# Performance work log

Hardware: AMD Instinct MI355X
Metric: run time of the kernel (lower is better)

The kernel has to match this reference:

```python
import jax, jax.numpy as jnp
import numpy as np
import math

HIDDEN = 2048
HEADS = 16
HEAD_DIM = HIDDEN // HEADS
RANK = HIDDEN // 2  # rank_ratio=0.5
B, S = 1, 4096


def setup_inputs() -> dict:
    key = jax.random.key(0)
    ks = jax.random.split(key, 10)
    sd = lambda fan_in: 1.0 / math.sqrt(fan_in)
    inp = {
        "hidden_states": jax.random.normal(ks[0], (B, S, HIDDEN), dtype=jnp.float32),
        "attention_mask": jnp.zeros((B, 1, S, S), dtype=jnp.float32),
        # low-rank projection weights; Linear weight shape is [out, in]
        "q_V": jax.random.uniform(ks[1], (RANK, HIDDEN), jnp.float32, -sd(HIDDEN), sd(HIDDEN)),
        "q_U": jax.random.uniform(ks[2], (HIDDEN, RANK), jnp.float32, -sd(RANK), sd(RANK)),
        "k_V": jax.random.uniform(ks[3], (RANK, HIDDEN), jnp.float32, -sd(HIDDEN), sd(HIDDEN)),
        "k_U": jax.random.uniform(ks[4], (HIDDEN, RANK), jnp.float32, -sd(RANK), sd(RANK)),
        "v_V": jax.random.uniform(ks[5], (RANK, HIDDEN), jnp.float32, -sd(HIDDEN), sd(HIDDEN)),
        "v_U": jax.random.uniform(ks[6], (HIDDEN, RANK), jnp.float32, -sd(RANK), sd(RANK)),
        "o_W": jax.random.uniform(ks[7], (HIDDEN, HIDDEN), jnp.float32, -sd(HIDDEN), sd(HIDDEN)),
        "o_b": jax.random.uniform(ks[8], (HIDDEN,), jnp.float32, -sd(HIDDEN), sd(HIDDEN)),
    }
    return inp


def _split_heads(x):
    # [B,S,HIDDEN] -> [B,H,S,Dh]
    b, s, _ = x.shape
    return x.reshape(b, s, HEADS, HEAD_DIM).transpose(0, 2, 1, 3)


def reference(hidden_states, attention_mask, q_V, q_U, k_V, k_U, v_V, v_U, o_W, o_b):
    # low-rank QKV: x @ V^T @ U^T
    q = _split_heads((hidden_states @ q_V.T) @ q_U.T)
    k = _split_heads((hidden_states @ k_V.T) @ k_U.T)
    v = _split_heads((hidden_states @ v_V.T) @ v_U.T)
    scores = jnp.einsum("bhqd,bhkd->bhqk", q, k) / math.sqrt(HEAD_DIM)
    scores = scores + attention_mask
    attn = jax.nn.softmax(scores, axis=-1)
    out = jnp.einsum("bhqk,bhkd->bhqd", attn, v)
    out = out.transpose(0, 2, 1, 3).reshape(hidden_states.shape[0], hidden_states.shape[1], HIDDEN)
    out = out @ o_W.T + o_b
    return out
```

## Files before the change

kernel.cpp:

```cpp
#include <hip/hip_runtime.h>

#define HIDDEN 2048
#define HEADS 16
#define HD 128
#define RANK 1024
#define SEQ 4096

typedef __bf16 bf16_t;
typedef __bf16 bf16x8 __attribute__((ext_vector_type(8)));
typedef __bf16 bf16x4 __attribute__((ext_vector_type(4)));
typedef float f32x4 __attribute__((ext_vector_type(4)));

#define MFMA_BF16(a, b, c) __builtin_amdgcn_mfma_f32_16x16x32_bf16((a), (b), (c), 0, 0, 0)

__device__ __forceinline__ void gload16(const bf16_t* g, bf16_t* l) {
  __builtin_amdgcn_global_load_lds(
      (const __attribute__((address_space(1))) unsigned int*)g,
      (__attribute__((address_space(3))) unsigned int*)l, 16, 0, 0);
}

struct CastSeg { const float* s; bf16_t* d; int n4; };
struct CastArgs { CastSeg seg[8]; };

__global__ __launch_bounds__(256) void cast_bf16_kernel(CastArgs a) {
  const int stride = gridDim.x * blockDim.x;
  const int tid0 = blockIdx.x * blockDim.x + threadIdx.x;
#pragma unroll
  for (int i = 0; i < 8; i++) {
    const float4* src = (const float4*)a.seg[i].s;
    bf16x4* dst = (bf16x4*)a.seg[i].d;
    const int n4 = a.seg[i].n4;
    for (int j = tid0; j < n4; j += stride) {
      float4 v = src[j];
      dst[j] = bf16x4{(bf16_t)v.x, (bf16_t)v.y, (bf16_t)v.z, (bf16_t)v.w};
    }
  }
}

template <int OUT_MODE>
__global__ __launch_bounds__(256) void gemm3(const bf16_t* __restrict__ A, int lda, int aOff,
                                             const bf16_t* __restrict__ W0,
                                             const bf16_t* __restrict__ W1,
                                             const bf16_t* __restrict__ W2,
                                             int nPerThird, int K,
                                             void* __restrict__ Cp, int ldc, size_t cOff,
                                             const float* __restrict__ bias, float s0,
                                             bf16_t* __restrict__ Ct) {
  __shared__ bf16_t As[128 * 32];
  __shared__ bf16_t Bs[128 * 32];
  const int tid = threadIdx.x, lane = tid & 63, wave = tid >> 6;
  const int wr = wave >> 1, wc = wave & 1, quad = lane >> 4, l15 = lane & 15;
  const int n0g = blockIdx.x * 128;
  const int third = n0g / nPerThird;
  const int n0 = n0g - third * nPerThird;
  const bf16_t* W = third == 0 ? W0 : (third == 1 ? W1 : W2);
  const bf16_t* Ab = A + (size_t)third * aOff;
  const int m0 = blockIdx.y * 128;
  const float sc = (third == 0) ? s0 : 1.f;

  f32x4 acc[4][4];
#pragma unroll
  for (int i = 0; i < 4; i++)
#pragma unroll
    for (int j = 0; j < 4; j++) acc[i][j] = f32x4{0.f, 0.f, 0.f, 0.f};

  const int KT = K >> 5;
  for (int kt = 0; kt < KT; ++kt) {
#pragma unroll
    for (int i = 0; i < 2; i++) {
      int slot = (wave * 2 + i) * 64 + lane;
      int row = slot >> 2, cp = slot & 3;
      int cl = cp ^ ((row >> 1) & 3);
      gload16(Ab + (size_t)(m0 + row) * lda + kt * 32 + cl * 8, As + (size_t)(wave * 2 + i) * 512);
    }
#pragma unroll
    for (int i = 0; i < 2; i++) {
      int slot = (wave * 2 + i) * 64 + lane;
      int row = slot >> 2, cp = slot & 3;
      int cl = cp ^ ((row >> 1) & 3);
      gload16(W + (size_t)(n0 + row) * K + kt * 32 + cl * 8, Bs + (size_t)(wave * 2 + i) * 512);
    }
    __syncthreads();

    bf16x8 af[4], bfr[4];
#pragma unroll
    for (int mt = 0; mt < 4; mt++) {
      int row = wr * 64 + mt * 16 + l15;
      int phys = quad ^ ((row >> 1) & 3);
      af[mt] = *reinterpret_cast<const bf16x8*>(As + row * 32 + phys * 8);
    }
#pragma unroll
    for (int nt = 0; nt < 4; nt++) {
      int row = wc * 64 + nt * 16 + l15;
      int phys = quad ^ ((row >> 1) & 3);
      bfr[nt] = *reinterpret_cast<const bf16x8*>(Bs + row * 32 + phys * 8);
    }
#pragma unroll
    for (int mt = 0; mt < 4; mt++)
#pragma unroll
      for (int nt = 0; nt < 4; nt++) acc[mt][nt] = MFMA_BF16(af[mt], bfr[nt], acc[mt][nt]);
    __syncthreads();
  }

  if constexpr (OUT_MODE == 2) {
    if (third == 2) {
#pragma unroll
      for (int nt = 0; nt < 4; nt++) {
        int col = n0 + wc * 64 + nt * 16 + l15;
#pragma unroll
        for (int mt = 0; mt < 4; mt++) {
          int rowb = m0 + wr * 64 + mt * 16 + quad * 4;
          bf16x4 tv = {(bf16_t)acc[mt][nt][0], (bf16_t)acc[mt][nt][1],
                       (bf16_t)acc[mt][nt][2], (bf16_t)acc[mt][nt][3]};
          *reinterpret_cast<bf16x4*>(Ct + (size_t)col * SEQ + rowb) = tv;
        }
      }
      return;
    }
  }

#pragma unroll
  for (int nt = 0; nt < 4; nt++) {
    int col = n0 + wc * 64 + nt * 16 + l15;
    float bv = 0.f;
    if constexpr (OUT_MODE == 1) bv = bias[col];
#pragma unroll
    for (int mt = 0; mt < 4; mt++) {
      int rowb = m0 + wr * 64 + mt * 16 + quad * 4;
#pragma unroll
      for (int r = 0; r < 4; r++) {
        float vx = acc[mt][nt][r];
        if constexpr (OUT_MODE == 1)
          ((float*)Cp + (size_t)third * cOff)[(size_t)(rowb + r) * ldc + col] = vx + bv;
        else
          ((bf16_t*)Cp + (size_t)third * cOff)[(size_t)(rowb + r) * ldc + col] = (bf16_t)(vx * sc);
      }
    }
  }
}

__global__ __launch_bounds__(256, 2) void attn_kernel(const bf16_t* __restrict__ qb,
                                                      const bf16_t* __restrict__ kb,
                                                      const bf16_t* __restrict__ vtp,
                                                      const float* __restrict__ mask,
                                                      bf16_t* __restrict__ ao) {
  __shared__ bf16_t Ks[2][64 * 128];
  __shared__ bf16_t Vs[3][128 * 64];
  const int tid = threadIdx.x, lane = tid & 63, w = tid >> 6;
  const int quad = lane >> 4, l15 = lane & 15;
  const int head = blockIdx.x, q0 = blockIdx.y * 128;
  const float LOG2E = 1.4426950408889634f;
  const int NT = SEQ / 64;

  bf16x8 qf[2][4];
#pragma unroll
  for (int qt = 0; qt < 2; qt++)
#pragma unroll
    for (int ks = 0; ks < 4; ks++)
      qf[qt][ks] = *reinterpret_cast<const bf16x8*>(
          qb + (size_t)(q0 + w * 32 + qt * 16 + l15) * HIDDEN + head * HD + ks * 32 + quad * 8);

  f32x4 O[8][2];
#pragma unroll
  for (int dt = 0; dt < 8; dt++)
#pragma unroll
    for (int qt = 0; qt < 2; qt++) O[dt][qt] = f32x4{0.f, 0.f, 0.f, 0.f};
  float lacc[2] = {0.f, 0.f};

  auto stageK = [&](int kt, int buf) {
#pragma unroll
    for (int i = 0; i < 4; i++) {
      int slot = (w * 4 + i) * 64 + lane;
      int row = slot >> 4, cp = slot & 15;
      int cl = cp ^ ((row & 3) | ((row & 8) >> 1));
      gload16(kb + (size_t)(kt * 64 + row) * HIDDEN + head * HD + cl * 8,
              &Ks[buf][(size_t)(w * 4 + i) * 512]);
    }
  };
  auto stageV = [&](int kt, int buf) {
#pragma unroll
    for (int i = 0; i < 4; i++) {
      int slot = (w * 4 + i) * 64 + lane;
      int row = slot >> 3, cp = slot & 7;
      int cl = cp ^ (row & 7);
      gload16(vtp + (size_t)(head * HD + row) * SEQ + kt * 64 + cl * 8,
              &Vs[buf][(size_t)(w * 4 + i) * 512]);
    }
  };

  const int sK = (l15 & 3) | (((l15 >> 2) & 1) << 2);
  const int rA0 = ((l15 >> 2) << 3) + (l15 & 3);

  f32x4 mv[2][2][2];
  auto loadMask = [&](int kt) {
#pragma unroll
    for (int kp = 0; kp < 2; kp++)
#pragma unroll
      for (int sub = 0; sub < 2; sub++)
#pragma unroll
        for (int qt = 0; qt < 2; qt++)
          mv[kp][sub][qt] = *reinterpret_cast<const f32x4*>(
              mask + (size_t)(q0 + w * 32 + qt * 16 + l15) * SEQ + kt * 64 + kp * 32 + quad * 8 +
              sub * 4);
  };

  f32x4 sacc[2][2][2];
  auto qkT = [&](int buf) {
#pragma unroll
    for (int kp = 0; kp < 2; kp++)
#pragma unroll
      for (int sub = 0; sub < 2; sub++)
#pragma unroll
        for (int qt = 0; qt < 2; qt++) sacc[kp][sub][qt] = f32x4{0.f, 0.f, 0.f, 0.f};
#pragma unroll
    for (int ks = 0; ks < 4; ks++) {
      int phys = (ks * 4 + quad) ^ sK;
#pragma unroll
      for (int kp = 0; kp < 2; kp++)
#pragma unroll
        for (int sub = 0; sub < 2; sub++) {
          int rowA = kp * 32 + sub * 4 + rA0;
          bf16x8 ak = *reinterpret_cast<const bf16x8*>(&Ks[buf][rowA * 128 + phys * 8]);
#pragma unroll
          for (int qt = 0; qt < 2; qt++)
            sacc[kp][sub][qt] = MFMA_BF16(ak, qf[qt][ks], sacc[kp][sub][qt]);
        }
    }
  };

  bf16x8 pf[2][2];
  auto softmaxF = [&]() {
#pragma unroll
    for (int kp = 0; kp < 2; kp++)
#pragma unroll
      for (int sub = 0; sub < 2; sub++)
#pragma unroll
        for (int qt = 0; qt < 2; qt++) {
          f32x4 e;
#pragma unroll
          for (int r = 0; r < 4; r++)
            e[r] = exp2f(sacc[kp][sub][qt][r] + mv[kp][sub][qt][r] * LOG2E);
          lacc[qt] += (e[0] + e[1]) + (e[2] + e[3]);
#pragma unroll
          for (int r = 0; r < 4; r++) pf[kp][qt][sub * 4 + r] = (bf16_t)e[r];
        }
  };

  auto pv = [&](const bf16_t* Vb) {
#pragma unroll
    for (int kp = 0; kp < 2; kp++)
#pragma unroll
      for (int dt = 0; dt < 8; dt++) {
        int row = dt * 16 + l15;
        int phys = (kp * 4 + quad) ^ (l15 & 7);
        bf16x8 av = *reinterpret_cast<const bf16x8*>(&Vb[row * 64 + phys * 8]);
#pragma unroll
        for (int qt = 0; qt < 2; qt++) O[dt][qt] = MFMA_BF16(av, pf[kp][qt], O[dt][qt]);
      }
  };

  stageK(0, 0);
  stageV(0, 0);
  stageK(1, 1);
  stageV(1, 1);
  loadMask(0);
  __syncthreads();
  qkT(0);

  int vb_pv = 0;
  int vb_st = 2;
  for (int t = 0; t < NT - 1; ++t) {
    softmaxF();
    __syncthreads();
    stageK(t + 2, t & 1);
    stageV(t + 2, vb_st);
    loadMask(t + 1);
    __builtin_amdgcn_s_setprio(1);
    qkT((t + 1) & 1);
    pv(&Vs[vb_pv][0]);
    __builtin_amdgcn_s_setprio(0);
    vb_pv = vb_pv == 2 ? 0 : vb_pv + 1;
    vb_st = vb_st == 2 ? 0 : vb_st + 1;
  }
  softmaxF();
  pv(&Vs[vb_pv][0]);

#pragma unroll
  for (int qt = 0; qt < 2; qt++) {
    float l = lacc[qt];
    l += __shfl_xor(l, 16, 64);
    l += __shfl_xor(l, 32, 64);
    lacc[qt] = 1.f / l;
  }
#pragma unroll
  for (int dt = 0; dt < 8; dt++)
#pragma unroll
    for (int qt = 0; qt < 2; qt++) {
      int q = q0 + w * 32 + qt * 16 + l15;
      int d = head * HD + dt * 16 + quad * 4;
      f32x4 o = O[dt][qt];
      bf16x4 ov = {(bf16_t)(o[0] * lacc[qt]), (bf16_t)(o[1] * lacc[qt]),
                   (bf16_t)(o[2] * lacc[qt]), (bf16_t)(o[3] * lacc[qt])};
      *reinterpret_cast<bf16x4*>(ao + (size_t)q * HIDDEN + d) = ov;
    }
}

extern "C" void kernel_launch(void* const* d_in, const int* in_sizes, int n_in,
                              void* d_out, int out_size, void* d_ws, size_t ws_size,
                              hipStream_t stream) {
  (void)in_sizes; (void)n_in; (void)out_size; (void)ws_size;
  const float* x = (const float*)d_in[0];
  const float* mask = (const float*)d_in[1];
  const float* qV = (const float*)d_in[2];
  const float* qU = (const float*)d_in[3];
  const float* kV = (const float*)d_in[4];
  const float* kU = (const float*)d_in[5];
  const float* vV = (const float*)d_in[6];
  const float* vU = (const float*)d_in[7];
  const float* oW = (const float*)d_in[8];
  const float* ob = (const float*)d_in[9];
  float* out = (float*)d_out;

  char* ws = (char*)d_ws;
  const size_t MB = 1ull << 20;
  bf16_t* xb  = (bf16_t*)(ws);
  bf16_t* tmp = (bf16_t*)(ws + 16 * MB);
  bf16_t* qkv = (bf16_t*)(ws + 40 * MB);
  bf16_t* qVb = (bf16_t*)(ws + 88 * MB);
  bf16_t* qUb = (bf16_t*)(ws + 92 * MB);
  bf16_t* kVb = (bf16_t*)(ws + 96 * MB);
  bf16_t* kUb = (bf16_t*)(ws + 100 * MB);
  bf16_t* vVb = (bf16_t*)(ws + 104 * MB);
  bf16_t* vUb = (bf16_t*)(ws + 108 * MB);
  bf16_t* oWb = (bf16_t*)(ws + 112 * MB);
  bf16_t* vt = qkv + 2 * (size_t)SEQ * HIDDEN;

  const float kQScale = 0.088388347648318447f * 1.4426950408889634f;

  CastArgs ca;
  ca.seg[0] = {x, xb, SEQ * HIDDEN / 4};
  ca.seg[1] = {qV, qVb, RANK * HIDDEN / 4};
  ca.seg[2] = {qU, qUb, HIDDEN * RANK / 4};
  ca.seg[3] = {kV, kVb, RANK * HIDDEN / 4};
  ca.seg[4] = {kU, kUb, HIDDEN * RANK / 4};
  ca.seg[5] = {vV, vVb, RANK * HIDDEN / 4};
  ca.seg[6] = {vU, vUb, HIDDEN * RANK / 4};
  ca.seg[7] = {oW, oWb, HIDDEN * HIDDEN / 4};
  cast_bf16_kernel<<<2048, 256, 0, stream>>>(ca);

  gemm3<0><<<dim3(24, 32), 256, 0, stream>>>(xb, HIDDEN, 0, qVb, kVb, vVb, RANK, HIDDEN,
                                             tmp, 3 * RANK, (size_t)RANK, nullptr, 1.f, nullptr);
  gemm3<2><<<dim3(48, 32), 256, 0, stream>>>(tmp, 3 * RANK, RANK, qUb, kUb, vUb, HIDDEN, RANK,
                                             qkv, HIDDEN, (size_t)SEQ * HIDDEN, nullptr,
                                             kQScale, vt);
  attn_kernel<<<dim3(HEADS, SEQ / 128), 256, 0, stream>>>(qkv, qkv + (size_t)SEQ * HIDDEN, vt,
                                                          mask, xb);
  gemm3<1><<<dim3(16, 32), 256, 0, stream>>>(xb, HIDDEN, 0, oWb, oWb, oWb, HIDDEN, HIDDEN,
                                             out, HIDDEN, 0, ob, 1.f, nullptr);
}
```

Measured before the change: 584.3 us.

## Interleave softmax exponentials with next tile's QK^T MFMAs and use fast exp2

The standalone softmax pass over the previous score tile is removed. Each slice of it now runs between the MFMA groups that compute the next tile's QK^T scores, so VALU exp work can overlap matrix-core work. The mask load for the next tile is moved after this fused step so the current mask is still available. The libm exp2f is also replaced with the hardware exp2 builtin. The cost is a second live set of score accumulators, which raises register pressure and may reduce occupancy.

Result: faster. 558.3 us (-4.4%).

```diff
diff --git a/kernel.cpp b/kernel.cpp
--- a/kernel.cpp
+++ b/kernel.cpp
@@ -205,6 +205,21 @@
   };
 
   f32x4 sacc[2][2][2];
+  bf16x8 pf[2][2];
+
+  auto smGroup = [&](int kp, int sub) {
+#pragma unroll
+    for (int qt = 0; qt < 2; qt++) {
+      f32x4 e;
+#pragma unroll
+      for (int r = 0; r < 4; r++)
+        e[r] = __builtin_amdgcn_exp2f(sacc[kp][sub][qt][r] + mv[kp][sub][qt][r] * LOG2E);
+      lacc[qt] += (e[0] + e[1]) + (e[2] + e[3]);
+#pragma unroll
+      for (int r = 0; r < 4; r++) pf[kp][qt][sub * 4 + r] = (bf16_t)e[r];
+    }
+  };
+
   auto qkT = [&](int buf) {
 #pragma unroll
     for (int kp = 0; kp < 2; kp++)
@@ -228,22 +243,35 @@
     }
   };
 
-  bf16x8 pf[2][2];
-  auto softmaxF = [&]() {
+  auto qkT_sm = [&](int buf) {
+    f32x4 ns[2][2][2];
 #pragma unroll
     for (int kp = 0; kp < 2; kp++)
 #pragma unroll
       for (int sub = 0; sub < 2; sub++)
 #pragma unroll
-        for (int qt = 0; qt < 2; qt++) {
-          f32x4 e;
-#pragma unroll
-          for (int r = 0; r < 4; r++)
-            e[r] = exp2f(sacc[kp][sub][qt][r] + mv[kp][sub][qt][r] * LOG2E);
-          lacc[qt] += (e[0] + e[1]) + (e[2] + e[3]);
-#pragma unroll
-          for (int r = 0; r < 4; r++) pf[kp][qt][sub * 4 + r] = (bf16_t)e[r];
+        for (int qt = 0; qt < 2; qt++) ns[kp][sub][qt] = f32x4{0.f, 0.f, 0.f, 0.f};
+#pragma unroll
+    for (int ks = 0; ks < 4; ks++) {
+      int phys = (ks * 4 + quad) ^ sK;
+#pragma unroll
+      for (int kp = 0; kp < 2; kp++)
+#pragma unroll
+        for (int sub = 0; sub < 2; sub++) {
+          int rowA = kp * 32 + sub * 4 + rA0;
+          bf16x8 ak = *reinterpret_cast<const bf16x8*>(&Ks[buf][rowA * 128 + phys * 8]);
+#pragma unroll
+          for (int qt = 0; qt < 2; qt++)
+            ns[kp][sub][qt] = MFMA_BF16(ak, qf[qt][ks], ns[kp][sub][qt]);
         }
+      smGroup(ks >> 1, ks & 1);
+    }
+#pragma unroll
+    for (int kp = 0; kp < 2; kp++)
+#pragma unroll
+      for (int sub = 0; sub < 2; sub++)
+#pragma unroll
+        for (int qt = 0; qt < 2; qt++) sacc[kp][sub][qt] = ns[kp][sub][qt];
   };
 
   auto pv = [&](const bf16_t* Vb) {
@@ -270,19 +298,23 @@
   int vb_pv = 0;
   int vb_st = 2;
   for (int t = 0; t < NT - 1; ++t) {
-    softmaxF();
     __syncthreads();
     stageK(t + 2, t & 1);
     stageV(t + 2, vb_st);
+    __builtin_amdgcn_s_setprio(1);
+    qkT_sm((t + 1) & 1);
+    __builtin_amdgcn_s_setprio(0);
     loadMask(t + 1);
     __builtin_amdgcn_s_setprio(1);
-    qkT((t + 1) & 1);
     pv(&Vs[vb_pv][0]);
     __builtin_amdgcn_s_setprio(0);
     vb_pv = vb_pv == 2 ? 0 : vb_pv + 1;
     vb_st = vb_st == 2 ? 0 : vb_st + 1;
   }
-  softmaxF();
+  smGroup(0, 0);
+  smGroup(0, 1);
+  smGroup(1, 0);
+  smGroup(1, 1);
   pv(&Vs[vb_pv][0]);
 
 #pragma unroll
```

## Split attention key tiles across two wave groups with LDS reduction of partial outputs

Applied to the files above, without the earlier changes.

The attention block grows to 512 threads, and the two groups of four waves each take half of every 64-key tile. Per-wave score and mask registers shrink, which should allow more waves in flight. Softmax for the previous tile is interleaved into the next QK^T MFMA loop, and the barrier becomes an explicit vmcnt wait. Partial O and row sums are combined through shared memory at the end, adding an extra reduction step and more LDS use.

Result: slower. 1.182 ms (+102.2%).

```diff
diff --git a/kernel.cpp b/kernel.cpp
--- a/kernel.cpp
+++ b/kernel.cpp
@@ -139,15 +139,23 @@
   }
 }
 
-__global__ __launch_bounds__(256, 2) void attn_kernel(const bf16_t* __restrict__ qb,
+__global__ __launch_bounds__(512, 4) void attn_kernel(const bf16_t* __restrict__ qb,
                                                       const bf16_t* __restrict__ kb,
                                                       const bf16_t* __restrict__ vtp,
                                                       const float* __restrict__ mask,
                                                       bf16_t* __restrict__ ao) {
-  __shared__ bf16_t Ks[2][64 * 128];
-  __shared__ bf16_t Vs[3][128 * 64];
+  __shared__ __align__(16) char smem[81920];
+  bf16_t* KsB = (bf16_t*)smem;
+  bf16_t* VsB = (bf16_t*)(smem + 32768);
+  float* osc = (float*)smem;
+  float* lsc = (float*)(smem + 65536);
+  auto Ks = [&](int b) { return KsB + b * (64 * 128); };
+  auto Vs = [&](int b) { return VsB + b * (128 * 64); };
+
   const int tid = threadIdx.x, lane = tid & 63, w = tid >> 6;
   const int quad = lane >> 4, l15 = lane & 15;
+  const int wq = w & 3;
+  const int kpc = w >> 2;
   const int head = blockIdx.x, q0 = blockIdx.y * 128;
   const float LOG2E = 1.4426950408889634f;
   const int NT = SEQ / 64;
@@ -158,7 +166,7 @@
 #pragma unroll
     for (int ks = 0; ks < 4; ks++)
       qf[qt][ks] = *reinterpret_cast<const bf16x8*>(
-          qb + (size_t)(q0 + w * 32 + qt * 16 + l15) * HIDDEN + head * HD + ks * 32 + quad * 8);
+          qb + (size_t)(q0 + wq * 32 + qt * 16 + l15) * HIDDEN + head * HD + ks * 32 + quad * 8);
 
   f32x4 O[8][2];
 #pragma unroll
@@ -169,94 +177,107 @@
 
   auto stageK = [&](int kt, int buf) {
 #pragma unroll
-    for (int i = 0; i < 4; i++) {
-      int slot = (w * 4 + i) * 64 + lane;
+    for (int i = 0; i < 2; i++) {
+      int slot = (w * 2 + i) * 64 + lane;
       int row = slot >> 4, cp = slot & 15;
       int cl = cp ^ ((row & 3) | ((row & 8) >> 1));
       gload16(kb + (size_t)(kt * 64 + row) * HIDDEN + head * HD + cl * 8,
-              &Ks[buf][(size_t)(w * 4 + i) * 512]);
+              Ks(buf) + (size_t)(w * 2 + i) * 512);
     }
   };
   auto stageV = [&](int kt, int buf) {
 #pragma unroll
-    for (int i = 0; i < 4; i++) {
-      int slot = (w * 4 + i) * 64 + lane;
+    for (int i = 0; i < 2; i++) {
+      int slot = (w * 2 + i) * 64 + lane;
       int row = slot >> 3, cp = slot & 7;
       int cl = cp ^ (row & 7);
       gload16(vtp + (size_t)(head * HD + row) * SEQ + kt * 64 + cl * 8,
-              &Vs[buf][(size_t)(w * 4 + i) * 512]);
+              Vs(buf) + (size_t)(w * 2 + i) * 512);
     }
   };
 
   const int sK = (l15 & 3) | (((l15 >> 2) & 1) << 2);
-  const int rA0 = ((l15 >> 2) << 3) + (l15 & 3);
-
-  f32x4 mv[2][2][2];
+  const int rA0 = kpc * 32 + ((l15 >> 2) << 3) + (l15 & 3);
+
+  f32x4 mv[2][2];
   auto loadMask = [&](int kt) {
 #pragma unroll
-    for (int kp = 0; kp < 2; kp++)
-#pragma unroll
-      for (int sub = 0; sub < 2; sub++)
-#pragma unroll
-        for (int qt = 0; qt < 2; qt++)
-          mv[kp][sub][qt] = *reinterpret_cast<const f32x4*>(
-              mask + (size_t)(q0 + w * 32 + qt * 16 + l15) * SEQ + kt * 64 + kp * 32 + quad * 8 +
-              sub * 4);
-  };
-
-  f32x4 sacc[2][2][2];
+    for (int sub = 0; sub < 2; sub++)
+#pragma unroll
+      for (int qt = 0; qt < 2; qt++)
+        mv[sub][qt] = *reinterpret_cast<const f32x4*>(
+            mask + (size_t)(q0 + wq * 32 + qt * 16 + l15) * SEQ + kt * 64 + kpc * 32 + quad * 8 +
+            sub * 4);
+  };
+
+  f32x4 sacc[2][2];
+  bf16x8 pf[2];
+
+  auto smOwn = [&](int sub) {
+#pragma unroll
+    for (int qt = 0; qt < 2; qt++) {
+      f32x4 e;
+#pragma unroll
+      for (int r = 0; r < 4; r++)
+        e[r] = __builtin_amdgcn_exp2f(sacc[sub][qt][r] + mv[sub][qt][r] * LOG2E);
+      lacc[qt] += (e[0] + e[1]) + (e[2] + e[3]);
+#pragma unroll
+      for (int r = 0; r < 4; r++) pf[qt][sub * 4 + r] = (bf16_t)e[r];
+    }
+  };
+
   auto qkT = [&](int buf) {
 #pragma unroll
-    for (int kp = 0; kp < 2; kp++)
-#pragma unroll
-      for (int sub = 0; sub < 2; sub++)
-#pragma unroll
-        for (int qt = 0; qt < 2; qt++) sacc[kp][sub][qt] = f32x4{0.f, 0.f, 0.f, 0.f};
+    for (int sub = 0; sub < 2; sub++)
+#pragma unroll
+      for (int qt = 0; qt < 2; qt++) sacc[sub][qt] = f32x4{0.f, 0.f, 0.f, 0.f};
 #pragma unroll
     for (int ks = 0; ks < 4; ks++) {
       int phys = (ks * 4 + quad) ^ sK;
 #pragma unroll
-      for (int kp = 0; kp < 2; kp++)
-#pragma unroll
-        for (int sub = 0; sub < 2; sub++) {
-          int rowA = kp * 32 + sub * 4 + rA0;
-          bf16x8 ak = *reinterpret_cast<const bf16x8*>(&Ks[buf][rowA * 128 + phys * 8]);
-#pragma unroll
-          for (int qt = 0; qt < 2; qt++)
-            sacc[kp][sub][qt] = MFMA_BF16(ak, qf[qt][ks], sacc[kp][sub][qt]);
-        }
-    }
-  };
-
-  bf16x8 pf[2][2];
-  auto softmaxF = [&]() {
-#pragma unroll
-    for (int kp = 0; kp < 2; kp++)
-#pragma unroll
-      for (int sub = 0; sub < 2; sub++)
-#pragma unroll
-        for (int qt = 0; qt < 2; qt++) {
-          f32x4 e;
-#pragma unroll
-          for (int r = 0; r < 4; r++)
-            e[r] = exp2f(sacc[kp][sub][qt][r] + mv[kp][sub][qt][r] * LOG2E);
-          lacc[qt] += (e[0] + e[1]) + (e[2] + e[3]);
-#pragma unroll
-          for (int r = 0; r < 4; r++) pf[kp][qt][sub * 4 + r] = (bf16_t)e[r];
-        }
+      for (int sub = 0; sub < 2; sub++) {
+        int rowA = sub * 4 + rA0;
+        bf16x8 ak = *reinterpret_cast<const bf16x8*>(Ks(buf) + rowA * 128 + phys * 8);
+#pragma unroll
+        for (int qt = 0; qt < 2; qt++) sacc[sub][qt] = MFMA_BF16(ak, qf[qt][ks], sacc[sub][qt]);
+      }
+    }
+  };
+
+  auto qkT_sm = [&](int buf) {
+    f32x4 ns[2][2];
+#pragma unroll
+    for (int sub = 0; sub < 2; sub++)
+#pragma unroll
+      for (int qt = 0; qt < 2; qt++) ns[sub][qt] = f32x4{0.f, 0.f, 0.f, 0.f};
+#pragma unroll
+    for (int ks = 0; ks < 4; ks++) {
+      int phys = (ks * 4 + quad) ^ sK;
+#pragma unroll
+      for (int sub = 0; sub < 2; sub++) {
+        int rowA = sub * 4 + rA0;
+        bf16x8 ak = *reinterpret_cast<const bf16x8*>(Ks(buf) + rowA * 128 + phys * 8);
+#pragma unroll
+        for (int qt = 0; qt < 2; qt++) ns[sub][qt] = MFMA_BF16(ak, qf[qt][ks], ns[sub][qt]);
+      }
+      if (ks == 1) smOwn(0);
+      if (ks == 3) smOwn(1);
+    }
+#pragma unroll
+    for (int sub = 0; sub < 2; sub++)
+#pragma unroll
+      for (int qt = 0; qt < 2; qt++) sacc[sub][qt] = ns[sub][qt];
   };
 
   auto pv = [&](const bf16_t* Vb) {
 #pragma unroll
-    for (int kp = 0; kp < 2; kp++)
-#pragma unroll
-      for (int dt = 0; dt < 8; dt++) {
-        int row = dt * 16 + l15;
-        int phys = (kp * 4 + quad) ^ (l15 & 7);
-        bf16x8 av = *reinterpret_cast<const bf16x8*>(&Vb[row * 64 + phys * 8]);
-#pragma unroll
-        for (int qt = 0; qt < 2; qt++) O[dt][qt] = MFMA_BF16(av, pf[kp][qt], O[dt][qt]);
-      }
+    for (int dt = 0; dt < 8; dt++) {
+      int row = dt * 16 + l15;
+      int phys = (kpc * 4 + quad) ^ (l15 & 7);
+      bf16x8 av = *reinterpret_cast<const bf16x8*>(&Vb[row * 64 + phys * 8]);
+#pragma unroll
+      for (int qt = 0; qt < 2; qt++) O[dt][qt] = MFMA_BF16(av, pf[qt], O[dt][qt]);
+    }
   };
 
   stageK(0, 0);
@@ -270,39 +291,56 @@
   int vb_pv = 0;
   int vb_st = 2;
   for (int t = 0; t < NT - 1; ++t) {
-    softmaxF();
-    __syncthreads();
+    asm volatile("s_waitcnt vmcnt(4) lgkmcnt(0)" ::: "memory");
+    __builtin_amdgcn_s_barrier();
+    __builtin_amdgcn_sched_barrier(0);
     stageK(t + 2, t & 1);
     stageV(t + 2, vb_st);
+    __builtin_amdgcn_sched_barrier(0);
     loadMask(t + 1);
     __builtin_amdgcn_s_setprio(1);
-    qkT((t + 1) & 1);
-    pv(&Vs[vb_pv][0]);
+    qkT_sm((t + 1) & 1);
+    pv(Vs(vb_pv));
     __builtin_amdgcn_s_setprio(0);
     vb_pv = vb_pv == 2 ? 0 : vb_pv + 1;
     vb_st = vb_st == 2 ? 0 : vb_st + 1;
   }
-  softmaxF();
-  pv(&Vs[vb_pv][0]);
-
-#pragma unroll
-  for (int qt = 0; qt < 2; qt++) {
-    float l = lacc[qt];
-    l += __shfl_xor(l, 16, 64);
-    l += __shfl_xor(l, 32, 64);
-    lacc[qt] = 1.f / l;
-  }
-#pragma unroll
-  for (int dt = 0; dt < 8; dt++)
+  smOwn(0);
+  smOwn(1);
+  pv(Vs(vb_pv));
+
+  __syncthreads();
+  if (kpc == 0) {
+#pragma unroll
+    for (int dt = 0; dt < 8; dt++)
+#pragma unroll
+      for (int qt = 0; qt < 2; qt++)
+        *reinterpret_cast<f32x4*>(&osc[(dt * 2 + qt) * 1024 + (wq * 64 + lane) * 4]) = O[dt][qt];
+    lsc[(wq * 64 + lane) * 2 + 0] = lacc[0];
+    lsc[(wq * 64 + lane) * 2 + 1] = lacc[1];
+  }
+  __syncthreads();
+  if (kpc == 1) {
 #pragma unroll
     for (int qt = 0; qt < 2; qt++) {
-      int q = q0 + w * 32 + qt * 16 + l15;
-      int d = head * HD + dt * 16 + quad * 4;
-      f32x4 o = O[dt][qt];
-      bf16x4 ov = {(bf16_t)(o[0] * lacc[qt]), (bf16_t)(o[1] * lacc[qt]),
-                   (bf16_t)(o[2] * lacc[qt]), (bf16_t)(o[3] * lacc[qt])};
-      *reinterpret_cast<bf16x4*>(ao + (size_t)q * HIDDEN + d) = ov;
-    }
+      float l = lacc[qt] + lsc[(wq * 64 + lane) * 2 + qt];
+      l += __shfl_xor(l, 16, 64);
+      l += __shfl_xor(l, 32, 64);
+      lacc[qt] = 1.f / l;
+    }
+#pragma unroll
+    for (int dt = 0; dt < 8; dt++)
+#pragma unroll
+      for (int qt = 0; qt < 2; qt++) {
+        f32x4 o = O[dt][qt] +
+                  *reinterpret_cast<const f32x4*>(&osc[(dt * 2 + qt) * 1024 + (wq * 64 + lane) * 4]);
+        int q = q0 + wq * 32 + qt * 16 + l15;
+        int d = head * HD + dt * 16 + quad * 4;
+        bf16x4 ov = {(bf16_t)(o[0] * lacc[qt]), (bf16_t)(o[1] * lacc[qt]),
+                     (bf16_t)(o[2] * lacc[qt]), (bf16_t)(o[3] * lacc[qt])};
+        *reinterpret_cast<bf16x4*>(ao + (size_t)q * HIDDEN + d) = ov;
+      }
+  }
 }
 
 extern "C" void kernel_launch(void* const* d_in, const int* in_sizes, int n_in,
@@ -353,7 +391,7 @@
   gemm3<2><<<dim3(48, 32), 256, 0, stream>>>(tmp, 3 * RANK, RANK, qUb, kUb, vUb, HIDDEN, RANK,
                                              qkv, HIDDEN, (size_t)SEQ * HIDDEN, nullptr,
                                              kQScale, vt);
-  attn_kernel<<<dim3(HEADS, SEQ / 128), 256, 0, stream>>>(qkv, qkv + (size_t)SEQ * HIDDEN, vt,
+  attn_kernel<<<dim3(HEADS, SEQ / 128), 512, 0, stream>>>(qkv, qkv + (size_t)SEQ * HIDDEN, vt,
                                                           mask, xb);
   gemm3<1><<<dim3(16, 32), 256, 0, stream>>>(xb, HIDDEN, 0, oWb, oWb, oWb, HIDDEN, HIDDEN,
                                              out, HIDDEN, 0, ob, 1.f, nullptr);
```
